# Performance work log

Measured on AMD Instinct MI355X. Metric: run time of the kernel, lower is better.

Reference implementation:

```python
import jax, jax.numpy as jnp
import numpy as np

BN_EPS = 1e-3  # Keras BatchNormalization default epsilon

def _bn(x, p):
    # p: [4, d] = gamma, beta, moving_mean, moving_var (inference-mode BN)
    g, b, m, v = p[0], p[1], p[2], p[3]
    return g * (x - m) * jax.lax.rsqrt(v + BN_EPS) + b

def _ffn_block(x, pbn, w, c):
    # BatchNorm -> Dropout(identity at inference) -> Dense(gelu, exact erf like tf.nn.gelu)
    return jax.nn.gelu(_bn(x, pbn) @ w + c, approximate=False)

def setup_inputs() -> dict:
    key = jax.random.key(0)
    ks = jax.random.split(key, 16)
    N, E, D, H = 100000, 1600000, 64, 64
    def bn_pack(k, d):
        k1, k2, k3, k4 = jax.random.split(k, 4)
        gamma = 1.0 + 0.1 * jax.random.normal(k1, (d,), jnp.float32)
        beta = 0.1 * jax.random.normal(k2, (d,), jnp.float32)
        mean = 0.05 * jax.random.normal(k3, (d,), jnp.float32)
        var = jax.random.uniform(k4, (d,), jnp.float32, 0.5, 1.5)
        return jnp.stack([gamma, beta, mean, var], axis=0)
    def dense(k, fan_in, fan_out):
        return (jax.random.normal(k, (fan_in, fan_out), jnp.float32) / np.sqrt(fan_in)).astype(jnp.float32)
    return {
        "x": jax.random.normal(ks[0], (N, D), jnp.float32),
        "edges": jax.random.randint(ks[1], (2, E), 0, N, jnp.int32),
        "ew": jax.random.uniform(ks[2], (E,), jnp.float32),
        "pbn1": bn_pack(ks[3], D),
        "pw1": dense(ks[4], D, H),
        "pc1": 0.01 * jax.random.normal(ks[5], (H,), jnp.float32),
        "pbn2": bn_pack(ks[6], H),
        "pw2": dense(ks[7], H, H),
        "pc2": 0.01 * jax.random.normal(ks[8], (H,), jnp.float32),
        "ubn1": bn_pack(ks[9], D + H),
        "uw1": dense(ks[10], D + H, H),
        "uc1": 0.01 * jax.random.normal(ks[11], (H,), jnp.float32),
        "ubn2": bn_pack(ks[12], H),
        "uw2": dense(ks[13], H, H),
        "uc2": 0.01 * jax.random.normal(ks[14], (H,), jnp.float32),
    }

def reference(x, edges, ew, pbn1, pw1, pc1, pbn2, pw2, pc2, ubn1, uw1, uc1, ubn2, uw2, uc2):
    N = x.shape[0]
    node_idx, nbr_idx = edges[0], edges[1]
    # gather neighbour representations -> prepare FFN -> edge-weight scaling
    nbr = x[nbr_idx]                                   # [E, D]
    h = _ffn_block(nbr, pbn1, pw1, pc1)                # [E, H]
    h = _ffn_block(h, pbn2, pw2, pc2)                  # [E, H]
    msgs = h * ew[:, None]
    # unsorted_segment_mean: sum / count (0 for empty segments)
    s = jax.ops.segment_sum(msgs, node_idx, num_segments=N)            # [N, H]
    cnt = jax.ops.segment_sum(jnp.ones_like(ew), node_idx, num_segments=N)
    agg = s / jnp.maximum(cnt, 1.0)[:, None]
    # combination_type='concat' -> update FFN
    hcat = jnp.concatenate([x, agg], axis=1)           # [N, D+H]
    out = _ffn_block(hcat, ubn1, uw1, uc1)
    out = _ffn_block(out, ubn2, uw2, uc2)              # [N, H]
    return out
```

## Files before the change

kernel.cpp:

```cpp
#include <hip/hip_runtime.h>
#include <hip/hip_bf16.h>
#include <hip/hip_fp16.h>

#define BN_EPS 1e-3f
#define GSH 6
#define GNODES 64
#define NB_MAX 1600
#define BIN_E 8192
#define CAP_SH 11
#define BKT_CAP 2048

typedef __attribute__((ext_vector_type(8))) short short8;
typedef __attribute__((ext_vector_type(4))) float f32x4;

__device__ __forceinline__ float gelu_exact(float v) {
    return 0.5f * v * (1.0f + erff(v * 0.70710678118654752440f));
}
__device__ __forceinline__ short f2b(float f) {
    __hip_bfloat16 h = __float2bfloat16(f);
    return *reinterpret_cast<short*>(&h);
}

union Y16 { uint4 u; __half2 h[4]; };

struct MatDesc {
    const float* bn; const float* W; const float* c;
    short* Wswz; float* cp; int K; int base;
};

__global__ void __launch_bounds__(256) prep_all(
    const float* pbn1, const float* pw1, const float* pc1,
    const float* pbn2, const float* pw2, const float* pc2,
    const float* ubn1, const float* uw1, const float* uc1,
    const float* ubn2, const float* uw2, const float* uc2,
    short* W1s, float* c1p, short* W2s, float* c2p,
    short* U1s, float* uc1p, short* U2s, float* uc2p,
    int* __restrict__ gcur, int NB) {
    __shared__ float red[4][64];
    const MatDesc md[4] = {
        {pbn1, pw1, pc1, W1s, c1p, 64, 0},
        {pbn2, pw2, pc2, W2s, c2p, 64, 4096},
        {ubn1, uw1, uc1, U1s, uc1p, 128, 8192},
        {ubn2, uw2, uc2, U2s, uc2p, 64, 16384},
    };
    const int bid = blockIdx.x;
    if (bid < 20) {
        for (int gidx = bid * 256 + threadIdx.x; gidx < 20480; gidx += 20 * 256) {
            int m = (gidx < 4096) ? 0 : (gidx < 8192) ? 1 : (gidx < 16384) ? 2 : 3;
            const MatDesc& d = md[m];
            int idx = gidx - d.base;
            int KC = d.K / 32;
            int j = idx & 7, lane = (idx >> 3) & 63, f = idx >> 9;
            int h = f % KC, t = f / KC;
            int k = h * 32 + (lane >> 4) * 8 + j;
            int col = t * 16 + (lane & 15);
            float s = d.bn[k] * rsqrtf(d.bn[3 * d.K + k] + BN_EPS);
            d.Wswz[idx] = f2b(s * d.W[k * 64 + col]);
        }
    } else if (bid < 24) {
        const MatDesc& d = md[bid - 20];
        const int j = threadIdx.x & 63, kk = threadIdx.x >> 6;
        const int chunk = d.K / 4;
        float acc = 0.f;
        for (int i = 0; i < chunk; ++i) {
            int k = kk * chunk + i;
            float s = d.bn[k] * rsqrtf(d.bn[3 * d.K + k] + BN_EPS);
            float t = d.bn[d.K + k] - d.bn[2 * d.K + k] * s;
            acc += t * d.W[k * 64 + j];
        }
        red[kk][j] = acc;
        __syncthreads();
        if (threadIdx.x < 64)
            d.cp[j] = d.c[j] + red[0][j] + red[1][j] + red[2][j] + red[3][j];
    } else {
        int i = (bid - 24) * 256 + threadIdx.x;
        if (i < NB) gcur[i] = i << CAP_SH;
    }
}

__global__ void __launch_bounds__(256) bin_ffn2(
    const int* __restrict__ node_idx, const int* __restrict__ nbr_idx,
    const float* __restrict__ ew, int* __restrict__ gcur,
    unsigned* __restrict__ es2,
    const float* __restrict__ X,
    const short* __restrict__ W1s, const float* __restrict__ c1,
    const short* __restrict__ W2s, const float* __restrict__ c2,
    __half* __restrict__ yh, int E, int NB, int NBLK, int N) {
    __shared__ int cntL[NB_MAX];
    __shared__ short Hs[4][16][72];
    const int tid = threadIdx.x;

    if (blockIdx.x < NBLK) {
        for (int i = tid; i < NB; i += 256) cntL[i] = 0;
        const int base = blockIdx.x * BIN_E;
        const int end = min(base + BIN_E, E);
        int nd[32];
        unsigned pl[32];
        bool vl[32];
#pragma unroll
        for (int j = 0; j < 32; ++j) {
            int e = base + tid + j * 256;
            vl[j] = e < end;
            int ee = vl[j] ? e : base;
            int n = node_idx[ee];
            unsigned q = (unsigned)(ew[ee] * 511.f + 0.5f);
            nd[j] = n;
            pl[j] = ((unsigned)nbr_idx[ee] << 15) |
                    ((unsigned)(n & (GNODES - 1)) << 9) | q;
        }
        __syncthreads();
#pragma unroll
        for (int j = 0; j < 32; ++j)
            if (vl[j]) atomicAdd(&cntL[nd[j] >> GSH], 1);
        __syncthreads();
        for (int i = tid; i < NB; i += 256) {
            int c = cntL[i];
            if (c) cntL[i] = atomicAdd(&gcur[i], c);
        }
        __syncthreads();
#pragma unroll
        for (int j = 0; j < 32; ++j) {
            if (vl[j]) {
                int b = nd[j] >> GSH;
                int s = atomicAdd(&cntL[b], 1);
                if (s < ((b + 1) << CAP_SH)) es2[s] = pl[j];
            }
        }
        return;
    }

    const int lane = tid & 63;
    const int wv = tid >> 6;
    const int lm = lane & 15, lh = lane >> 4;
    const int r0 = (blockIdx.x - NBLK) * 64 + wv * 16;
    if (r0 >= N) return;
    const int rowA = min(r0 + lm, N - 1);

    short8 a[2];
    {
        const float* xp = X + (size_t)rowA * 64 + lh * 8;
#pragma unroll
        for (int h = 0; h < 2; ++h) {
            float4 u0 = *reinterpret_cast<const float4*>(xp + h * 32);
            float4 u1 = *reinterpret_cast<const float4*>(xp + h * 32 + 4);
            short8 r;
            r[0] = f2b(u0.x); r[1] = f2b(u0.y); r[2] = f2b(u0.z); r[3] = f2b(u0.w);
            r[4] = f2b(u1.x); r[5] = f2b(u1.y); r[6] = f2b(u1.z); r[7] = f2b(u1.w);
            a[h] = r;
        }
    }

#pragma unroll
    for (int t = 0; t < 4; ++t) {
        float cb = c1[t * 16 + lm];
        f32x4 acc = {cb, cb, cb, cb};
#pragma unroll
        for (int h = 0; h < 2; ++h) {
            short8 b = *reinterpret_cast<const short8*>(
                W1s + ((size_t)(t * 2 + h) * 64 + lane) * 8);
            acc = __builtin_amdgcn_mfma_f32_16x16x32_bf16(a[h], b, acc, 0, 0, 0);
        }
#pragma unroll
        for (int q = 0; q < 4; ++q)
            Hs[wv][4 * lh + q][t * 16 + lm] = f2b(gelu_exact(acc[q]));
    }

    short8 a2[2];
#pragma unroll
    for (int h = 0; h < 2; ++h)
        a2[h] = *reinterpret_cast<const short8*>(&Hs[wv][lm][h * 32 + lh * 8]);

#pragma unroll
    for (int t = 0; t < 4; ++t) {
        float cb = c2[t * 16 + lm];
        f32x4 acc = {cb, cb, cb, cb};
#pragma unroll
        for (int h = 0; h < 2; ++h) {
            short8 b = *reinterpret_cast<const short8*>(
                W2s + ((size_t)(t * 2 + h) * 64 + lane) * 8);
            acc = __builtin_amdgcn_mfma_f32_16x16x32_bf16(a2[h], b, acc, 0, 0, 0);
        }
#pragma unroll
        for (int q = 0; q < 4; ++q) {
            int row = r0 + 4 * lh + q;
            if (row < N)
                yh[(size_t)row * 64 + t * 16 + lm] = __float2half(gelu_exact(acc[q]));
        }
    }
}

__global__ void __launch_bounds__(256) agg_uffn(
    const __half* __restrict__ yh, const unsigned* __restrict__ es2,
    const int* __restrict__ gcur, const float* __restrict__ X,
    const short* __restrict__ U1s, const float* __restrict__ c1,
    const short* __restrict__ U2s, const float* __restrict__ c2,
    float* __restrict__ out, int N) {
    __shared__ unsigned pay[BKT_CAP];
    __shared__ short S[4][16][72];
    __shared__ int offW[4][GNODES];
    __shared__ int curW[4][GNODES];
    __shared__ int offL[GNODES + 1];
    const int tid = threadIdx.x;
    const int lane = tid & 63;
    const int wv = tid >> 6;
    const int b = blockIdx.x;
    const int s0 = b << CAP_SH;
    const int tot = min(gcur[b] - s0, BKT_CAP);

    unsigned ec[8];
    bool val[8];
#pragma unroll
    for (int c = 0; c < 8; ++c) {
        int i = tid + c * 256;
        val[c] = i < tot;
        ec[c] = val[c] ? es2[s0 + i] : 0u;
    }
    offW[wv][lane] = 0;
    __syncthreads();
#pragma unroll
    for (int c = 0; c < 8; ++c)
        if (val[c]) atomicAdd(&offW[wv][(ec[c] >> 9) & (GNODES - 1)], 1);
    __syncthreads();
    if (wv == 0) {
        int c0 = offW[0][lane], c1w = offW[1][lane];
        int c2w = offW[2][lane], c3 = offW[3][lane];
        int v = c0 + c1w + c2w + c3;
        const int orig = v;
#pragma unroll
        for (int d = 1; d < 64; d <<= 1) {
            int n = __shfl_up(v, (unsigned)d, 64);
            if (lane >= d) v += n;
        }
        int ex = v - orig;
        offL[lane] = ex;
        if (lane == 63) offL[64] = v;
        curW[0][lane] = ex;
        curW[1][lane] = ex + c0;
        curW[2][lane] = ex + c0 + c1w;
        curW[3][lane] = ex + c0 + c1w + c2w;
    }
    __syncthreads();
#pragma unroll
    for (int c = 0; c < 8; ++c) {
        if (val[c]) {
            int slot = atomicAdd(&curW[wv][(ec[c] >> 9) & (GNODES - 1)], 1);
            pay[slot] = ec[c];
        }
    }
    __syncthreads();

    const int g = lane >> 3, lg = lane & 7;
    {
        const int nA = wv * 16 + g, nB = nA + 8;
        const int loA = offL[nA], hiA = offL[nA + 1];
        const int loB = offL[nB], hiB = offL[nB + 1];
        const int lenA = hiA - loA, lenB = hiB - loB;
        const int kmax = max(lenA, lenB);
        __half2 accA[4], accB[4];
        const __half2 z = __float2half2_rn(0.f);
#pragma unroll
        for (int j = 0; j < 4; ++j) { accA[j] = z; accB[j] = z; }
        for (int k = 0; k < kmax; k += 2) {
#pragma unroll
            for (int u = 0; u < 2; ++u) {
                const int kk = k + u;
                {
                    const bool v = kk < lenA;
                    unsigned e = pay[max(min(loA + kk, hiA - 1), 0)];
                    float wf = v ? (float)(e & 511u) * (1.f / 511.f) : 0.f;
                    __half2 w = __half2half2(__float2half(wf));
                    Y16 y;
                    y.u = *reinterpret_cast<const uint4*>(
                        yh + (size_t)(e >> 15) * 64 + lg * 8);
#pragma unroll
                    for (int j = 0; j < 4; ++j) accA[j] = __hfma2(w, y.h[j], accA[j]);
                }
                {
                    const bool v = kk < lenB;
                    unsigned e = pay[max(min(loB + kk, hiB - 1), 0)];
                    float wf = v ? (float)(e & 511u) * (1.f / 511.f) : 0.f;
                    __half2 w = __half2half2(__float2half(wf));
                    Y16 y;
                    y.u = *reinterpret_cast<const uint4*>(
                        yh + (size_t)(e >> 15) * 64 + lg * 8);
#pragma unroll
                    for (int j = 0; j < 4; ++j) accB[j] = __hfma2(w, y.h[j], accB[j]);
                }
            }
        }
        float rcA = 1.f / fmaxf((float)lenA, 1.f);
        float rcB = 1.f / fmaxf((float)lenB, 1.f);
        short8 oA, oB;
#pragma unroll
        for (int j = 0; j < 4; ++j) {
            oA[2 * j]     = f2b(__low2float(accA[j]) * rcA);
            oA[2 * j + 1] = f2b(__high2float(accA[j]) * rcA);
            oB[2 * j]     = f2b(__low2float(accB[j]) * rcB);
            oB[2 * j + 1] = f2b(__high2float(accB[j]) * rcB);
        }
        *reinterpret_cast<short8*>(&S[wv][g][lg * 8]) = oA;
        *reinterpret_cast<short8*>(&S[wv][g + 8][lg * 8]) = oB;
    }

    const int lm = lane & 15, lh = lane >> 4;
    const int r0 = b * 64 + wv * 16;
    if (r0 >= N) return;
    const int rowA = min(r0 + lm, N - 1);

    short8 a[4];
    {
        const float* xp = X + (size_t)rowA * 64 + lh * 8;
#pragma unroll
        for (int h = 0; h < 2; ++h) {
            float4 u0 = *reinterpret_cast<const float4*>(xp + h * 32);
            float4 u1 = *reinterpret_cast<const float4*>(xp + h * 32 + 4);
            short8 r;
            r[0] = f2b(u0.x); r[1] = f2b(u0.y); r[2] = f2b(u0.z); r[3] = f2b(u0.w);
            r[4] = f2b(u1.x); r[5] = f2b(u1.y); r[6] = f2b(u1.z); r[7] = f2b(u1.w);
            a[h] = r;
        }
#pragma unroll
        for (int h = 0; h < 2; ++h)
            a[2 + h] = *reinterpret_cast<const short8*>(&S[wv][lm][h * 32 + lh * 8]);
    }

#pragma unroll
    for (int t = 0; t < 4; ++t) {
        float cb = c1[t * 16 + lm];
        f32x4 acc = {cb, cb, cb, cb};
#pragma unroll
        for (int h = 0; h < 4; ++h) {
            short8 bb = *reinterpret_cast<const short8*>(
                U1s + ((size_t)(t * 4 + h) * 64 + lane) * 8);
            acc = __builtin_amdgcn_mfma_f32_16x16x32_bf16(a[h], bb, acc, 0, 0, 0);
        }
#pragma unroll
        for (int q = 0; q < 4; ++q)
            S[wv][4 * lh + q][t * 16 + lm] = f2b(gelu_exact(acc[q]));
    }

    short8 a2[2];
#pragma unroll
    for (int h = 0; h < 2; ++h)
        a2[h] = *reinterpret_cast<const short8*>(&S[wv][lm][h * 32 + lh * 8]);

#pragma unroll
    for (int t = 0; t < 4; ++t) {
        float cb = c2[t * 16 + lm];
        f32x4 acc = {cb, cb, cb, cb};
#pragma unroll
        for (int h = 0; h < 2; ++h) {
            short8 bb = *reinterpret_cast<const short8*>(
                U2s + ((size_t)(t * 2 + h) * 64 + lane) * 8);
            acc = __builtin_amdgcn_mfma_f32_16x16x32_bf16(a2[h], bb, acc, 0, 0, 0);
        }
#pragma unroll
        for (int q = 0; q < 4; ++q) {
            int row = r0 + 4 * lh + q;
            if (row < N)
                out[(size_t)row * 64 + t * 16 + lm] = gelu_exact(acc[q]);
        }
    }
}

extern "C" void kernel_launch(void* const* d_in, const int* in_sizes, int n_in,
                              void* d_out, int out_size, void* d_ws, size_t ws_size,
                              hipStream_t stream) {
    const float* x    = (const float*)d_in[0];
    const int*   edges= (const int*)d_in[1];
    const float* ew   = (const float*)d_in[2];
    const float* pbn1 = (const float*)d_in[3];
    const float* pw1  = (const float*)d_in[4];
    const float* pc1  = (const float*)d_in[5];
    const float* pbn2 = (const float*)d_in[6];
    const float* pw2  = (const float*)d_in[7];
    const float* pc2  = (const float*)d_in[8];
    const float* ubn1 = (const float*)d_in[9];
    const float* uw1  = (const float*)d_in[10];
    const float* uc1  = (const float*)d_in[11];
    const float* ubn2 = (const float*)d_in[12];
    const float* uw2  = (const float*)d_in[13];
    const float* uc2  = (const float*)d_in[14];
    float* out = (float*)d_out;

    const int N = in_sizes[0] / 64;
    const int E = in_sizes[2];
    const int* node_idx = edges;
    const int* nbr_idx  = edges + E;
    const int NB = (N + GNODES - 1) / GNODES;
    const int NBLK = (E + BIN_E - 1) / BIN_E;
    const int FBLK = (N + 63) / 64;

    char* p = (char*)d_ws;
    auto alloc = [&](size_t bytes) {
        char* q = p;
        p += (bytes + 255) & ~(size_t)255;
        return q;
    };
    __half*   yh   = (__half*)alloc((size_t)N * 64 * 2);
    unsigned* es2  = (unsigned*)alloc((size_t)NB * BKT_CAP * 4);
    int*      gcur = (int*)alloc((size_t)NB * 4);
    short*    W1s  = (short*)alloc(4096 * 2);
    short*    W2s  = (short*)alloc(4096 * 2);
    short*    U1s  = (short*)alloc(8192 * 2);
    short*    U2s  = (short*)alloc(4096 * 2);
    float*    c1p  = (float*)alloc(64 * 4);
    float*    c2p  = (float*)alloc(64 * 4);
    float*    uc1p = (float*)alloc(64 * 4);
    float*    uc2p = (float*)alloc(64 * 4);

    prep_all<<<32, 256, 0, stream>>>(pbn1, pw1, pc1, pbn2, pw2, pc2,
                                     ubn1, uw1, uc1, ubn2, uw2, uc2,
                                     W1s, c1p, W2s, c2p, U1s, uc1p, U2s, uc2p,
                                     gcur, NB);
    bin_ffn2<<<NBLK + FBLK, 256, 0, stream>>>(node_idx, nbr_idx, ew, gcur, es2,
                                              x, W1s, c1p, W2s, c2p, yh,
                                              E, NB, NBLK, N);
    agg_uffn<<<NB, 256, 0, stream>>>(yh, es2, gcur, x, U1s, uc1p, U2s, uc2p, out, N);
}
```

Baseline: 96.08 us.

## Split edge binning by bucket slice so each block writes a subset of buckets

The binning phase now gives each 16K-edge range to 8 blocks. Each block handles only the buckets whose index modulo 8 matches its slice, so it keeps a much smaller shared counter array. The aim is to make each block's writes into es2 more local and less scattered, to shrink the LDS footprint, and to launch more blocks. In exchange, every block rereads node_idx for its whole range twice, which multiplies index traffic by 8 (largely served from L2). Register-held payload arrays are also replaced by plain loops.

```diff
diff --git a/kernel.cpp b/kernel.cpp
--- a/kernel.cpp
+++ b/kernel.cpp
@@ -6,7 +6,9 @@
 #define GSH 6
 #define GNODES 64
 #define NB_MAX 1600
-#define BIN_E 8192
+#define BIN_E 16384
+#define SPLIT 8
+#define NSL_MAX 200
 #define CAP_SH 11
 #define BKT_CAP 2048
 
@@ -85,45 +87,39 @@
     const float* __restrict__ X,
     const short* __restrict__ W1s, const float* __restrict__ c1,
     const short* __restrict__ W2s, const float* __restrict__ c2,
-    __half* __restrict__ yh, int E, int NB, int NBLK, int N) {
-    __shared__ int cntL[NB_MAX];
+    __half* __restrict__ yh, int E, int NB, int NBIN, int N) {
+    __shared__ int cntS[NSL_MAX];
     __shared__ short Hs[4][16][72];
     const int tid = threadIdx.x;
 
-    if (blockIdx.x < NBLK) {
-        for (int i = tid; i < NB; i += 256) cntL[i] = 0;
-        const int base = blockIdx.x * BIN_E;
+    if (blockIdx.x < NBIN) {
+        const int range = blockIdx.x / SPLIT;
+        const int slice = blockIdx.x % SPLIT;
+        const int base = range * BIN_E;
         const int end = min(base + BIN_E, E);
-        int nd[32];
-        unsigned pl[32];
-        bool vl[32];
-#pragma unroll
-        for (int j = 0; j < 32; ++j) {
-            int e = base + tid + j * 256;
-            vl[j] = e < end;
-            int ee = vl[j] ? e : base;
-            int n = node_idx[ee];
-            unsigned q = (unsigned)(ew[ee] * 511.f + 0.5f);
-            nd[j] = n;
-            pl[j] = ((unsigned)nbr_idx[ee] << 15) |
-                    ((unsigned)(n & (GNODES - 1)) << 9) | q;
-        }
+        const int nsl = (NB + SPLIT - 1) / SPLIT;
+        for (int i = tid; i < nsl; i += 256) cntS[i] = 0;
         __syncthreads();
-#pragma unroll
-        for (int j = 0; j < 32; ++j)
-            if (vl[j]) atomicAdd(&cntL[nd[j] >> GSH], 1);
+        for (int e = base + tid; e < end; e += 256) {
+            int b = node_idx[e] >> GSH;
+            if ((b & (SPLIT - 1)) == slice) atomicAdd(&cntS[b >> 3], 1);
+        }
         __syncthreads();
-        for (int i = tid; i < NB; i += 256) {
-            int c = cntL[i];
-            if (c) cntL[i] = atomicAdd(&gcur[i], c);
+        for (int i = tid; i < nsl; i += 256) {
+            int b = i * SPLIT + slice;
+            int c = cntS[i];
+            if (c && b < NB) cntS[i] = atomicAdd(&gcur[b], c);
         }
         __syncthreads();
-#pragma unroll
-        for (int j = 0; j < 32; ++j) {
-            if (vl[j]) {
-                int b = nd[j] >> GSH;
-                int s = atomicAdd(&cntL[b], 1);
-                if (s < ((b + 1) << CAP_SH)) es2[s] = pl[j];
+        for (int e = base + tid; e < end; e += 256) {
+            int n = node_idx[e];
+            int b = n >> GSH;
+            if ((b & (SPLIT - 1)) == slice) {
+                unsigned q = (unsigned)(ew[e] * 511.f + 0.5f);
+                unsigned pl = ((unsigned)nbr_idx[e] << 15) |
+                              ((unsigned)(n & (GNODES - 1)) << 9) | q;
+                int s = atomicAdd(&cntS[b >> 3], 1);
+                if (s < ((b + 1) << CAP_SH)) es2[s] = pl;
             }
         }
         return;
@@ -132,7 +128,7 @@
     const int lane = tid & 63;
     const int wv = tid >> 6;
     const int lm = lane & 15, lh = lane >> 4;
-    const int r0 = (blockIdx.x - NBLK) * 64 + wv * 16;
+    const int r0 = (blockIdx.x - NBIN) * 64 + wv * 16;
     if (r0 >= N) return;
     const int rowA = min(r0 + lm, N - 1);
 
@@ -388,7 +384,8 @@
     const int* node_idx = edges;
     const int* nbr_idx  = edges + E;
     const int NB = (N + GNODES - 1) / GNODES;
-    const int NBLK = (E + BIN_E - 1) / BIN_E;
+    const int NRANGE = (E + BIN_E - 1) / BIN_E;
+    const int NBIN = NRANGE * SPLIT;
     const int FBLK = (N + 63) / 64;
 
     char* p = (char*)d_ws;
@@ -413,8 +410,8 @@
                                      ubn1, uw1, uc1, ubn2, uw2, uc2,
                                      W1s, c1p, W2s, c2p, U1s, uc1p, U2s, uc2p,
                                      gcur, NB);
-    bin_ffn2<<<NBLK + FBLK, 256, 0, stream>>>(node_idx, nbr_idx, ew, gcur, es2,
+    bin_ffn2<<<NBIN + FBLK, 256, 0, stream>>>(node_idx, nbr_idx, ew, gcur, es2,
                                               x, W1s, c1p, W2s, c2p, yh,
-                                              E, NB, NBLK, N);
+                                              E, NB, NBIN, N);
     agg_uffn<<<NB, 256, 0, stream>>>(yh, es2, gcur, x, U1s, uc1p, U2s, uc2p, out, N);
 }
```

After: 149.2 us. 1.55x slower.
